# Optimization experiments

Measured on AMD Instinct MI355X. Metric: run time of the kernel, lower is better.

Reference implementation:

```python
import jax, jax.numpy as jnp
import numpy as np

DIM = 1024
HEADS = 16
HEAD_DIM = DIM // HEADS
SCALE = HEAD_DIM ** -0.5


def setup_inputs() -> dict:
    key = jax.random.key(0)
    ks = jax.random.split(key, 9)
    b, n, m = 4, 1024, 1024
    x = jax.random.normal(ks[0], (b, n, DIM), dtype=jnp.float32)
    context = jax.random.normal(ks[1], (b, m, DIM), dtype=jnp.float32)
    mask = jax.random.randint(ks[2], (b, n, 32, 32), 0, 2, dtype=jnp.int32)
    s = DIM ** -0.5
    Wq = jax.random.normal(ks[3], (DIM, DIM), dtype=jnp.float32) * s
    bq = jnp.zeros((DIM,), dtype=jnp.float32)
    Wkv = jax.random.normal(ks[4], (DIM, 2 * DIM), dtype=jnp.float32) * s
    bkv = jnp.zeros((2 * DIM,), dtype=jnp.float32)
    Wp = jax.random.normal(ks[5], (DIM, DIM), dtype=jnp.float32) * s
    bp = jnp.zeros((DIM,), dtype=jnp.float32)
    return {"x": x, "context": context, "mask": mask,
            "Wq": Wq, "bq": bq, "Wkv": Wkv, "bkv": bkv, "Wp": Wp, "bp": bp}


def reference(x, context, mask, Wq, bq, Wkv, bkv, Wp, bp):
    b, n, _ = x.shape
    m = context.shape[1]
    h, d = HEADS, HEAD_DIM
    # projections
    q = (x @ Wq + bq).reshape(b, n, h, d).transpose(0, 2, 1, 3)       # [b,h,n,d]
    kv = (context @ Wkv + bkv).reshape(b, m, 2, h, d)
    k = kv[:, :, 0].transpose(0, 2, 1, 3)                              # [b,h,m,d]
    v = kv[:, :, 1].transpose(0, 2, 1, 3)                              # [b,h,m,d]
    dots = jnp.einsum('bhnd,bhmd->bhnm', q, k) * SCALE                 # [b,h,n,m]
    # mask: [b,n,H,W] -> [b,1,n,m]; masked_fill where mask == 0
    mflat = mask.reshape(b, n, m)[:, None]                             # [b,1,n,m]
    dots = jnp.where(mflat == 0, -jnp.inf, dots)
    attn = jax.nn.softmax(dots, axis=-1)
    out = jnp.einsum('bhnm,bhmd->bhnd', attn, v)
    out = out.transpose(0, 2, 1, 3).reshape(b, n, h * d)
    return out @ Wp + bp
```

## Files before the change

### kernel.cpp

```cpp
#include <hip/hip_runtime.h>
#include <type_traits>

typedef __bf16 bf16;
typedef __bf16 bf16x8 __attribute__((ext_vector_type(8)));
typedef float f32x4 __attribute__((ext_vector_type(4)));
typedef unsigned long long u64;

#define MFMA16(a, b, c) __builtin_amdgcn_mfma_f32_16x16x32_bf16(a, b, c, 0, 0, 0)

__global__ __launch_bounds__(256)
void transpose_weights_k(const float* __restrict__ Wq,
                         const float* __restrict__ Wkv,
                         const float* __restrict__ Wp,
                         bf16* __restrict__ BqkvT, bf16* __restrict__ WpT) {
  const int ct = blockIdx.x, rt = blockIdx.y;
  const float* src;
  bf16* dst;
  int C, c0, drow0;
  if (ct < 16) {
    src = Wq; C = 1024; c0 = ct * 64; dst = BqkvT; drow0 = c0;
  } else if (ct < 48) {
    src = Wkv; C = 2048; c0 = (ct - 16) * 64; dst = BqkvT; drow0 = 1024 + c0;
  } else {
    src = Wp; C = 1024; c0 = (ct - 48) * 64; dst = WpT; drow0 = c0;
  }
  __shared__ bf16 T[64][72];
  const int tid = threadIdx.x;
  const int r0 = rt * 64;
#pragma unroll
  for (int i = 0; i < 2; ++i) {
    int c = i * 256 + tid;
    int row = c >> 3, col = (c & 7) * 8;
    const float* sp = &src[(size_t)(r0 + row) * C + c0 + col];
    f32x4 a0 = *(const f32x4*)sp;
    f32x4 a1 = *(const f32x4*)(sp + 4);
    bf16x8 t;
#pragma unroll
    for (int j = 0; j < 4; ++j) { t[j] = (bf16)a0[j]; t[4 + j] = (bf16)a1[j]; }
    *(bf16x8*)&T[row][col] = t;
  }
  __syncthreads();
#pragma unroll
  for (int i = 0; i < 2; ++i) {
    int c = i * 256 + tid;
    int orow = c >> 3, ocol = (c & 7) * 8;
    bf16x8 v;
#pragma unroll
    for (int j = 0; j < 8; ++j) v[j] = T[ocol + j][orow];
    *(bf16x8*)&dst[(size_t)(drow0 + orow) * 1024 + r0 + ocol] = v;
  }
}

__global__ __launch_bounds__(256)
void maskpack_k(const int* __restrict__ mask, u64* __restrict__ out) {
  const int idx = blockIdx.x * 256 + threadIdx.x;
  const int4* p = (const int4*)(mask + (size_t)idx * 64);
  u64 v = 0;
#pragma unroll
  for (int i = 0; i < 16; ++i) {
    int4 m = p[i];
    v |= (u64)(m.x != 0) << (4 * i);
    v |= (u64)(m.y != 0) << (4 * i + 1);
    v |= (u64)(m.z != 0) << (4 * i + 2);
    v |= (u64)(m.w != 0) << (4 * i + 3);
  }
  out[idx] = v;
}

template <int EPI, typename TA>
__global__ __launch_bounds__(256)
void gemm64x128(const TA* __restrict__ A0, const TA* __restrict__ A1,
                const bf16* __restrict__ Bt, const float* __restrict__ bias0,
                const float* __restrict__ bias1, bf16* __restrict__ oq,
                bf16* __restrict__ ok, bf16* __restrict__ ovt,
                float* __restrict__ out0f, int K) {
  __shared__ bf16 As[64][72];
  __shared__ bf16 Bs[128][72];
  const int tid = threadIdx.x;
  const int lane = tid & 63;
  const int w = tid >> 6;
  const int wm = (w >> 1) * 32, wn = (w & 1) * 64;
  const int l15 = lane & 15, l4 = lane >> 4;
  const int n0g = blockIdx.x * 128;
  const int m0 = blockIdx.y * 64;

  const TA* A = (EPI == 1 && n0g >= 1024) ? A1 : A0;

  const int ar = tid >> 2, ac0 = (tid & 3) * 16;
  const int br = tid >> 1, bc0 = (tid & 1) * 32;

  f32x4 acc[2][4] = {};

  for (int kk = 0; kk < K; kk += 64) {
    if constexpr (std::is_same_v<TA, float>) {
      const float* ap = &A[(size_t)(m0 + ar) * K + kk + ac0];
#pragma unroll
      for (int half = 0; half < 2; ++half) {
        f32x4 a0 = *(const f32x4*)(ap + half * 8);
        f32x4 a1 = *(const f32x4*)(ap + half * 8 + 4);
        bf16x8 t;
#pragma unroll
        for (int j = 0; j < 4; ++j) { t[j] = (bf16)a0[j]; t[4 + j] = (bf16)a1[j]; }
        *(bf16x8*)&As[ar][ac0 + half * 8] = t;
      }
    } else {
      const bf16* ap = &A[(size_t)(m0 + ar) * K + kk + ac0];
      *(bf16x8*)&As[ar][ac0] = *(const bf16x8*)ap;
      *(bf16x8*)&As[ar][ac0 + 8] = *(const bf16x8*)(ap + 8);
    }
    {
      const bf16* bp = &Bt[(size_t)(n0g + br) * K + kk + bc0];
#pragma unroll
      for (int half = 0; half < 4; ++half)
        *(bf16x8*)&Bs[br][bc0 + half * 8] = *(const bf16x8*)(bp + half * 8);
    }
    __syncthreads();
#pragma unroll
    for (int ks = 0; ks < 2; ++ks) {
      bf16x8 af[2], bfr[4];
#pragma unroll
      for (int i = 0; i < 2; ++i)
        af[i] = *(const bf16x8*)&As[wm + i * 16 + l15][ks * 32 + l4 * 8];
#pragma unroll
      for (int j = 0; j < 4; ++j)
        bfr[j] = *(const bf16x8*)&Bs[wn + j * 16 + l15][ks * 32 + l4 * 8];
#pragma unroll
      for (int i = 0; i < 2; ++i)
#pragma unroll
        for (int j = 0; j < 4; ++j)
          acc[i][j] = MFMA16(af[i], bfr[j], acc[i][j]);
    }
    __syncthreads();
  }

  const float SCALE2 = 0.18033688011112042f;
#pragma unroll
  for (int j = 0; j < 4; ++j) {
    const int col = n0g + wn + j * 16 + l15;
    float bc;
    if (EPI == 1) bc = (col < 1024) ? bias0[col] : bias1[col - 1024];
    else bc = bias0[col];
#pragma unroll
    for (int i = 0; i < 2; ++i) {
#pragma unroll
      for (int r = 0; r < 4; ++r) {
        const int row = m0 + wm + i * 16 + l4 * 4 + r;
        const float v = acc[i][j][r] + bc;
        if (EPI == 0) {
          out0f[(size_t)row * 1024 + col] = v;
        } else {
          const int b = row >> 10, n = row & 1023;
          if (col < 1024) {
            const int h = col >> 6, d = col & 63;
            oq[(((size_t)(b * 16 + h)) * 1024 + n) * 64 + d] =
                (bf16)(v * SCALE2);
          } else {
            const int ckv = col - 1024;
            const int s = ckv >> 10, c2 = ckv & 1023;
            const int h = c2 >> 6, d = c2 & 63;
            if (s == 0)
              ok[(((size_t)(b * 16 + h)) * 1024 + n) * 64 + d] = (bf16)v;
            else
              ovt[(((size_t)(b * 16 + h)) * 64 + d) * 1024 + n] = (bf16)v;
          }
        }
      }
    }
  }
}

__global__ __launch_bounds__(256)
void attn_kernel(const bf16* __restrict__ q, const bf16* __restrict__ k,
                 const bf16* __restrict__ vT, const u64* __restrict__ maskbits,
                 bf16* __restrict__ ao) {
  const int ntile = blockIdx.x;
  const int bh = blockIdx.y;
  const int b = bh >> 4, h = bh & 15;
  const int tid = threadIdx.x;
  const int lane = tid & 63;
  const int w = tid >> 6;
  const int l15 = lane & 15, l4 = lane >> 4;

  __shared__ bf16 Ks[64][72];
  __shared__ bf16 Vts[64][72];
  __shared__ bf16 Pw[4][16][72];

  const size_t base = (size_t)bh * 65536;
  const int nrow0 = ntile * 64 + w * 16;

  bf16x8 qf[2];
#pragma unroll
  for (int ks = 0; ks < 2; ++ks)
    qf[ks] =
        *(const bf16x8*)&q[base + (size_t)(nrow0 + l15) * 64 + ks * 32 + l4 * 8];

  f32x4 o[4] = {};
  float lsum[4] = {0.0f, 0.0f, 0.0f, 0.0f};

  const u64* mb = maskbits + (size_t)(b * 1024 + nrow0) * 16;

  for (int mt = 0; mt < 16; ++mt) {
#pragma unroll
    for (int i = 0; i < 2; ++i) {
      int c = i * 256 + tid;
      int row = c >> 3, col = (c & 7) * 8;
      *(bf16x8*)&Ks[row][col] =
          *(const bf16x8*)&k[base + (size_t)(mt * 64 + row) * 64 + col];
      *(bf16x8*)&Vts[row][col] =
          *(const bf16x8*)&vT[base + (size_t)row * 1024 + mt * 64 + col];
    }
    __syncthreads();

    f32x4 s[4];
#pragma unroll
    for (int sub = 0; sub < 4; ++sub) s[sub] = f32x4{-12.f, -12.f, -12.f, -12.f};
#pragma unroll
    for (int ks = 0; ks < 2; ++ks) {
#pragma unroll
      for (int sub = 0; sub < 4; ++sub) {
        bf16x8 bfr = *(const bf16x8*)&Ks[sub * 16 + l15][ks * 32 + l4 * 8];
        s[sub] = MFMA16(qf[ks], bfr, s[sub]);
      }
    }

    u64 wbits[4];
#pragma unroll
    for (int r = 0; r < 4; ++r) wbits[r] = mb[(size_t)(l4 * 4 + r) * 16 + mt];

#pragma unroll
    for (int sub = 0; sub < 4; ++sub) {
#pragma unroll
      for (int r = 0; r < 4; ++r) {
        float p = exp2f(s[sub][r]);
        p = ((wbits[r] >> (sub * 16 + l15)) & 1) ? p : 0.0f;
        lsum[r] += p;
        Pw[w][l4 * 4 + r][sub * 16 + l15] = (bf16)p;
      }
    }

#pragma unroll
    for (int ks = 0; ks < 2; ++ks) {
      bf16x8 af = *(const bf16x8*)&Pw[w][l15][ks * 32 + l4 * 8];
#pragma unroll
      for (int sub = 0; sub < 4; ++sub) {
        bf16x8 bfr = *(const bf16x8*)&Vts[sub * 16 + l15][ks * 32 + l4 * 8];
        o[sub] = MFMA16(af, bfr, o[sub]);
      }
    }
    __syncthreads();
  }

  float inv[4];
#pragma unroll
  for (int r = 0; r < 4; ++r) {
    float t = lsum[r];
#pragma unroll
    for (int d = 1; d < 16; d <<= 1) t += __shfl_xor(t, d);
    inv[r] = 1.0f / t;
  }

#pragma unroll
  for (int sub = 0; sub < 4; ++sub) {
#pragma unroll
    for (int r = 0; r < 4; ++r) {
      const int n = nrow0 + l4 * 4 + r;
      const size_t idx =
          ((size_t)(b * 1024 + n)) * 1024 + h * 64 + sub * 16 + l15;
      ao[idx] = (bf16)(o[sub][r] * inv[r]);
    }
  }
}

extern "C" void kernel_launch(void* const* d_in, const int* in_sizes, int n_in,
                              void* d_out, int out_size, void* d_ws,
                              size_t ws_size, hipStream_t stream) {
  const float* x = (const float*)d_in[0];
  const float* context = (const float*)d_in[1];
  const int* mask = (const int*)d_in[2];
  const float* Wq = (const float*)d_in[3];
  const float* bq = (const float*)d_in[4];
  const float* Wkv = (const float*)d_in[5];
  const float* bkv = (const float*)d_in[6];
  const float* Wp = (const float*)d_in[7];
  const float* bp = (const float*)d_in[8];
  float* out = (float*)d_out;

  char* ws = (char*)d_ws;
  bf16* BqkvT = (bf16*)(ws);
  u64* maskbits = (u64*)(ws);
  bf16* WpT = (bf16*)(ws + (6ull << 20));
  bf16* qw = (bf16*)(ws + (8ull << 20));
  bf16* kw = (bf16*)(ws + (16ull << 20));
  bf16* vtw = (bf16*)(ws + (24ull << 20));
  bf16* aow = (bf16*)(ws + (32ull << 20));

  const dim3 blk(256);

  transpose_weights_k<<<dim3(64, 16), blk, 0, stream>>>(Wq, Wkv, Wp, BqkvT,
                                                        WpT);

  gemm64x128<1, float><<<dim3(24, 64), blk, 0, stream>>>(
      x, context, BqkvT, bq, bkv, qw, kw, vtw, nullptr, 1024);

  maskpack_k<<<dim3(256), blk, 0, stream>>>(mask, maskbits);

  attn_kernel<<<dim3(16, 64), blk, 0, stream>>>(qw, kw, vtw, maskbits, aow);

  gemm64x128<0, bf16><<<dim3(8, 64), blk, 0, stream>>>(
      aow, nullptr, WpT, bp, nullptr, nullptr, nullptr, nullptr, out, 1024);
}
```

Before: 249.6 us.

## Use direct global-to-LDS loads and larger QKV GEMM tiles with bf16 context precast

```diff
diff --git a/kernel.cpp b/kernel.cpp
--- a/kernel.cpp
+++ b/kernel.cpp
@@ -1,5 +1,4 @@
 #include <hip/hip_runtime.h>
-#include <type_traits>
 
 typedef __bf16 bf16;
 typedef __bf16 bf16x8 __attribute__((ext_vector_type(8)));
@@ -8,12 +7,30 @@
 
 #define MFMA16(a, b, c) __builtin_amdgcn_mfma_f32_16x16x32_bf16(a, b, c, 0, 0, 0)
 
+__device__ __forceinline__ void gl_lds16(const void* g, void* l) {
+  __builtin_amdgcn_global_load_lds(
+      (const __attribute__((address_space(1))) unsigned int*)g,
+      (__attribute__((address_space(3))) unsigned int*)l, 16, 0, 0);
+}
+
+__global__ __launch_bounds__(256)
+void cvt_f32_bf16_k(const float* __restrict__ src, bf16* __restrict__ dst) {
+  const size_t i = ((size_t)blockIdx.x * 256 + threadIdx.x) * 8;
+  f32x4 a0 = *(const f32x4*)(src + i);
+  f32x4 a1 = *(const f32x4*)(src + i + 4);
+  bf16x8 t;
+#pragma unroll
+  for (int j = 0; j < 4; ++j) { t[j] = (bf16)a0[j]; t[4 + j] = (bf16)a1[j]; }
+  *(bf16x8*)(dst + i) = t;
+}
+
 __global__ __launch_bounds__(256)
 void transpose_weights_k(const float* __restrict__ Wq,
                          const float* __restrict__ Wkv,
                          const float* __restrict__ Wp,
-                         bf16* __restrict__ BqkvT, bf16* __restrict__ WpT) {
-  const int ct = blockIdx.x, rt = blockIdx.y;
+                         bf16* __restrict__ BqkvT, bf16* __restrict__ WpT,
+                         int ct_off) {
+  const int ct = blockIdx.x + ct_off, rt = blockIdx.y;
   const float* src;
   bf16* dst;
   int C, c0, drow0;
@@ -67,52 +84,125 @@
   out[idx] = v;
 }
 
-template <int EPI, typename TA>
-__global__ __launch_bounds__(256)
-void gemm64x128(const TA* __restrict__ A0, const TA* __restrict__ A1,
-                const bf16* __restrict__ Bt, const float* __restrict__ bias0,
-                const float* __restrict__ bias1, bf16* __restrict__ oq,
-                bf16* __restrict__ ok, bf16* __restrict__ ovt,
-                float* __restrict__ out0f, int K) {
-  __shared__ bf16 As[64][72];
-  __shared__ bf16 Bs[128][72];
+__global__ __launch_bounds__(256)
+void gemm_qkv(const float* __restrict__ xf, const bf16* __restrict__ cb,
+              const bf16* __restrict__ Bt, const float* __restrict__ bq,
+              const float* __restrict__ bkv, bf16* __restrict__ oq,
+              bf16* __restrict__ ok, bf16* __restrict__ ovt) {
+  __shared__ bf16 As[128][64];
+  __shared__ bf16 Bs[128][64];
+  const int tid = threadIdx.x;
+  const int lane = tid & 63;
+  const int w = tid >> 6;
+  const int wm = (w >> 1) * 64, wn = (w & 1) * 64;
+  const int l15 = lane & 15, l4 = lane >> 4;
+  const int lrow = lane >> 3, lcol = (lane & 7) * 8;
+  const int n0g = blockIdx.x * 128;
+  const int m0 = blockIdx.y * 128;
+  const bool qside = (n0g < 1024);
+
+  const int ar = tid >> 1, ac0 = (tid & 1) * 32;
+
+  f32x4 acc[4][4] = {};
+
+  for (int kk = 0; kk < 1024; kk += 64) {
+#pragma unroll
+    for (int it = 0; it < 4; ++it) {
+      const int r = w * 32 + it * 8;
+      gl_lds16(&Bt[(size_t)(n0g + r + lrow) * 1024 + kk + lcol], &Bs[r][0]);
+    }
+    if (qside) {
+      const float* ap = &xf[(size_t)(m0 + ar) * 1024 + kk + ac0];
+#pragma unroll
+      for (int h = 0; h < 4; ++h) {
+        f32x4 a0 = *(const f32x4*)(ap + h * 8);
+        f32x4 a1 = *(const f32x4*)(ap + h * 8 + 4);
+        bf16x8 t;
+#pragma unroll
+        for (int j = 0; j < 4; ++j) { t[j] = (bf16)a0[j]; t[4 + j] = (bf16)a1[j]; }
+        *(bf16x8*)&As[ar][ac0 + h * 8] = t;
+      }
+    } else {
+#pragma unroll
+      for (int it = 0; it < 4; ++it) {
+        const int r = w * 32 + it * 8;
+        gl_lds16(&cb[(size_t)(m0 + r + lrow) * 1024 + kk + lcol], &As[r][0]);
+      }
+    }
+    __syncthreads();
+#pragma unroll
+    for (int ks = 0; ks < 2; ++ks) {
+      bf16x8 af[4], bfr[4];
+#pragma unroll
+      for (int i = 0; i < 4; ++i)
+        af[i] = *(const bf16x8*)&As[wm + i * 16 + l15][ks * 32 + l4 * 8];
+#pragma unroll
+      for (int j = 0; j < 4; ++j)
+        bfr[j] = *(const bf16x8*)&Bs[wn + j * 16 + l15][ks * 32 + l4 * 8];
+#pragma unroll
+      for (int i = 0; i < 4; ++i)
+#pragma unroll
+        for (int j = 0; j < 4; ++j)
+          acc[i][j] = MFMA16(af[i], bfr[j], acc[i][j]);
+    }
+    __syncthreads();
+  }
+
+  const float SCALE2 = 0.18033688011112042f;
+#pragma unroll
+  for (int j = 0; j < 4; ++j) {
+    const int col = n0g + wn + j * 16 + l15;
+    const float bc = (col < 1024) ? bq[col] : bkv[col - 1024];
+#pragma unroll
+    for (int i = 0; i < 4; ++i) {
+#pragma unroll
+      for (int r = 0; r < 4; ++r) {
+        const int row = m0 + wm + i * 16 + l4 * 4 + r;
+        const float v = acc[i][j][r] + bc;
+        const int b = row >> 10, n = row & 1023;
+        if (col < 1024) {
+          const int h = col >> 6, d = col & 63;
+          oq[(((size_t)(b * 16 + h)) * 1024 + n) * 64 + d] = (bf16)(v * SCALE2);
+        } else {
+          const int ckv = col - 1024;
+          const int s = ckv >> 10, c2 = ckv & 1023;
+          const int h = c2 >> 6, d = c2 & 63;
+          if (s == 0)
+            ok[(((size_t)(b * 16 + h)) * 1024 + n) * 64 + d] = (bf16)v;
+          else
+            ovt[(((size_t)(b * 16 + h)) * 64 + d) * 1024 + n] = (bf16)v;
+        }
+      }
+    }
+  }
+}
+
+__global__ __launch_bounds__(256)
+void gemm_op(const bf16* __restrict__ A, const bf16* __restrict__ Bt,
+             const float* __restrict__ bias, float* __restrict__ out) {
+  __shared__ bf16 As[64][64];
+  __shared__ bf16 Bs[128][64];
   const int tid = threadIdx.x;
   const int lane = tid & 63;
   const int w = tid >> 6;
   const int wm = (w >> 1) * 32, wn = (w & 1) * 64;
   const int l15 = lane & 15, l4 = lane >> 4;
-  const int n0g = blockIdx.x * 128;
+  const int lrow = lane >> 3, lcol = (lane & 7) * 8;
+  const int n0 = blockIdx.x * 128;
   const int m0 = blockIdx.y * 64;
 
-  const TA* A = (EPI == 1 && n0g >= 1024) ? A1 : A0;
-
-  const int ar = tid >> 2, ac0 = (tid & 3) * 16;
-  const int br = tid >> 1, bc0 = (tid & 1) * 32;
-
   f32x4 acc[2][4] = {};
 
-  for (int kk = 0; kk < K; kk += 64) {
-    if constexpr (std::is_same_v<TA, float>) {
-      const float* ap = &A[(size_t)(m0 + ar) * K + kk + ac0];
-#pragma unroll
-      for (int half = 0; half < 2; ++half) {
-        f32x4 a0 = *(const f32x4*)(ap + half * 8);
-        f32x4 a1 = *(const f32x4*)(ap + half * 8 + 4);
-        bf16x8 t;
-#pragma unroll
-        for (int j = 0; j < 4; ++j) { t[j] = (bf16)a0[j]; t[4 + j] = (bf16)a1[j]; }
-        *(bf16x8*)&As[ar][ac0 + half * 8] = t;
-      }
-    } else {
-      const bf16* ap = &A[(size_t)(m0 + ar) * K + kk + ac0];
-      *(bf16x8*)&As[ar][ac0] = *(const bf16x8*)ap;
-      *(bf16x8*)&As[ar][ac0 + 8] = *(const bf16x8*)(ap + 8);
-    }
-    {
-      const bf16* bp = &Bt[(size_t)(n0g + br) * K + kk + bc0];
-#pragma unroll
-      for (int half = 0; half < 4; ++half)
-        *(bf16x8*)&Bs[br][bc0 + half * 8] = *(const bf16x8*)(bp + half * 8);
+  for (int kk = 0; kk < 1024; kk += 64) {
+#pragma unroll
+    for (int it = 0; it < 4; ++it) {
+      const int r = w * 32 + it * 8;
+      gl_lds16(&Bt[(size_t)(n0 + r + lrow) * 1024 + kk + lcol], &Bs[r][0]);
+    }
+#pragma unroll
+    for (int it = 0; it < 2; ++it) {
+      const int r = w * 16 + it * 8;
+      gl_lds16(&A[(size_t)(m0 + r + lrow) * 1024 + kk + lcol], &As[r][0]);
     }
     __syncthreads();
 #pragma unroll
@@ -133,37 +223,16 @@
     __syncthreads();
   }
 
-  const float SCALE2 = 0.18033688011112042f;
 #pragma unroll
   for (int j = 0; j < 4; ++j) {
-    const int col = n0g + wn + j * 16 + l15;
-    float bc;
-    if (EPI == 1) bc = (col < 1024) ? bias0[col] : bias1[col - 1024];
-    else bc = bias0[col];
+    const int col = n0 + wn + j * 16 + l15;
+    const float bc = bias[col];
 #pragma unroll
     for (int i = 0; i < 2; ++i) {
 #pragma unroll
       for (int r = 0; r < 4; ++r) {
         const int row = m0 + wm + i * 16 + l4 * 4 + r;
-        const float v = acc[i][j][r] + bc;
-        if (EPI == 0) {
-          out0f[(size_t)row * 1024 + col] = v;
-        } else {
-          const int b = row >> 10, n = row & 1023;
-          if (col < 1024) {
-            const int h = col >> 6, d = col & 63;
-            oq[(((size_t)(b * 16 + h)) * 1024 + n) * 64 + d] =
-                (bf16)(v * SCALE2);
-          } else {
-            const int ckv = col - 1024;
-            const int s = ckv >> 10, c2 = ckv & 1023;
-            const int h = c2 >> 6, d = c2 & 63;
-            if (s == 0)
-              ok[(((size_t)(b * 16 + h)) * 1024 + n) * 64 + d] = (bf16)v;
-            else
-              ovt[(((size_t)(b * 16 + h)) * 64 + d) * 1024 + n] = (bf16)v;
-          }
-        }
+        out[(size_t)row * 1024 + col] = acc[i][j][r] + bc;
       }
     }
   }
@@ -286,26 +355,30 @@
   float* out = (float*)d_out;
 
   char* ws = (char*)d_ws;
-  bf16* BqkvT = (bf16*)(ws);
-  u64* maskbits = (u64*)(ws);
-  bf16* WpT = (bf16*)(ws + (6ull << 20));
-  bf16* qw = (bf16*)(ws + (8ull << 20));
-  bf16* kw = (bf16*)(ws + (16ull << 20));
-  bf16* vtw = (bf16*)(ws + (24ull << 20));
-  bf16* aow = (bf16*)(ws + (32ull << 20));
+  bf16* cb = (bf16*)(ws);
+  bf16* aow = (bf16*)(ws);
+  bf16* BqkvT = (bf16*)(ws + (8ull << 20));
+  u64* maskbits = (u64*)(ws + (8ull << 20));
+  bf16* WpT = (bf16*)(ws + (9ull << 20));
+  bf16* qw = (bf16*)(ws + (14ull << 20));
+  bf16* kw = (bf16*)(ws + (22ull << 20));
+  bf16* vtw = (bf16*)(ws + (30ull << 20));
 
   const dim3 blk(256);
 
-  transpose_weights_k<<<dim3(64, 16), blk, 0, stream>>>(Wq, Wkv, Wp, BqkvT,
-                                                        WpT);
-
-  gemm64x128<1, float><<<dim3(24, 64), blk, 0, stream>>>(
-      x, context, BqkvT, bq, bkv, qw, kw, vtw, nullptr, 1024);
+  cvt_f32_bf16_k<<<dim3(2048), blk, 0, stream>>>(context, cb);
+
+  transpose_weights_k<<<dim3(48, 16), blk, 0, stream>>>(Wq, Wkv, Wp, BqkvT,
+                                                        WpT, 0);
+
+  gemm_qkv<<<dim3(24, 32), blk, 0, stream>>>(x, cb, BqkvT, bq, bkv, qw, kw,
+                                             vtw);
 
   maskpack_k<<<dim3(256), blk, 0, stream>>>(mask, maskbits);
+  transpose_weights_k<<<dim3(16, 16), blk, 0, stream>>>(Wq, Wkv, Wp, BqkvT,
+                                                        WpT, 48);
 
   attn_kernel<<<dim3(16, 64), blk, 0, stream>>>(qw, kw, vtw, maskbits, aow);
 
-  gemm64x128<0, bf16><<<dim3(8, 64), blk, 0, stream>>>(
-      aow, nullptr, WpT, bp, nullptr, nullptr, nullptr, nullptr, out, 1024);
-}
+  gemm_op<<<dim3(8, 64), blk, 0, stream>>>(aow, WpT, bp, out);
+}
```

Measured after the change: 269.3 us. 7.9% more time.

## Merge prep kernels and use direct global-to-LDS loads with XOR-swizzled GEMM tiles

Applied to the files above, without the earlier changes.

```diff
diff --git a/kernel.cpp b/kernel.cpp
--- a/kernel.cpp
+++ b/kernel.cpp
@@ -1,5 +1,4 @@
 #include <hip/hip_runtime.h>
-#include <type_traits>
 
 typedef __bf16 bf16;
 typedef __bf16 bf16x8 __attribute__((ext_vector_type(8)));
@@ -8,12 +7,35 @@
 
 #define MFMA16(a, b, c) __builtin_amdgcn_mfma_f32_16x16x32_bf16(a, b, c, 0, 0, 0)
 
+__device__ __forceinline__ void gl_lds16(const void* g, void* l) {
+  __builtin_amdgcn_global_load_lds(
+      (const __attribute__((address_space(1))) unsigned int*)g,
+      (__attribute__((address_space(3))) unsigned int*)l, 16, 0, 0);
+}
+
 __global__ __launch_bounds__(256)
-void transpose_weights_k(const float* __restrict__ Wq,
-                         const float* __restrict__ Wkv,
-                         const float* __restrict__ Wp,
-                         bf16* __restrict__ BqkvT, bf16* __restrict__ WpT) {
-  const int ct = blockIdx.x, rt = blockIdx.y;
+void prep_k(const float* __restrict__ Wq, const float* __restrict__ Wkv,
+            const float* __restrict__ Wp, const int* __restrict__ mask,
+            bf16* __restrict__ BqkvT, bf16* __restrict__ WpT,
+            u64* __restrict__ maskbits) {
+  const int bx = blockIdx.x;
+  const int tid = threadIdx.x;
+  if (bx >= 1024) {
+    const int idx = (bx - 1024) * 256 + tid;
+    const int4* p = (const int4*)(mask + (size_t)idx * 64);
+    u64 v = 0;
+#pragma unroll
+    for (int i = 0; i < 16; ++i) {
+      int4 m = p[i];
+      v |= (u64)(m.x != 0) << (4 * i);
+      v |= (u64)(m.y != 0) << (4 * i + 1);
+      v |= (u64)(m.z != 0) << (4 * i + 2);
+      v |= (u64)(m.w != 0) << (4 * i + 3);
+    }
+    maskbits[idx] = v;
+    return;
+  }
+  const int ct = bx >> 4, rt = bx & 15;
   const float* src;
   bf16* dst;
   int C, c0, drow0;
@@ -25,7 +47,6 @@
     src = Wp; C = 1024; c0 = (ct - 48) * 64; dst = WpT; drow0 = c0;
   }
   __shared__ bf16 T[64][72];
-  const int tid = threadIdx.x;
   const int r0 = rt * 64;
 #pragma unroll
   for (int i = 0; i < 2; ++i) {
@@ -51,79 +72,68 @@
   }
 }
 
+template <int EPI>
 __global__ __launch_bounds__(256)
-void maskpack_k(const int* __restrict__ mask, u64* __restrict__ out) {
-  const int idx = blockIdx.x * 256 + threadIdx.x;
-  const int4* p = (const int4*)(mask + (size_t)idx * 64);
-  u64 v = 0;
-#pragma unroll
-  for (int i = 0; i < 16; ++i) {
-    int4 m = p[i];
-    v |= (u64)(m.x != 0) << (4 * i);
-    v |= (u64)(m.y != 0) << (4 * i + 1);
-    v |= (u64)(m.z != 0) << (4 * i + 2);
-    v |= (u64)(m.w != 0) << (4 * i + 3);
-  }
-  out[idx] = v;
-}
-
-template <int EPI, typename TA>
-__global__ __launch_bounds__(256)
-void gemm64x128(const TA* __restrict__ A0, const TA* __restrict__ A1,
-                const bf16* __restrict__ Bt, const float* __restrict__ bias0,
-                const float* __restrict__ bias1, bf16* __restrict__ oq,
-                bf16* __restrict__ ok, bf16* __restrict__ ovt,
-                float* __restrict__ out0f, int K) {
-  __shared__ bf16 As[64][72];
-  __shared__ bf16 Bs[128][72];
+void gemm_sw(const float* __restrict__ Af0, const float* __restrict__ Af1,
+             const bf16* __restrict__ Ab, const bf16* __restrict__ Bt,
+             const float* __restrict__ bias0, const float* __restrict__ bias1,
+             bf16* __restrict__ oq, bf16* __restrict__ ok,
+             bf16* __restrict__ ovt, float* __restrict__ outf) {
+  __shared__ bf16 As[64][64];
+  __shared__ bf16 Bs[128][64];
   const int tid = threadIdx.x;
   const int lane = tid & 63;
   const int w = tid >> 6;
   const int wm = (w >> 1) * 32, wn = (w & 1) * 64;
   const int l15 = lane & 15, l4 = lane >> 4;
-  const int n0g = blockIdx.x * 128;
+  const int lrow = lane >> 3;
+  const int scol = ((lane & 7) ^ (lrow & 7)) * 8;
+  const int n0 = blockIdx.x * 128;
   const int m0 = blockIdx.y * 64;
 
-  const TA* A = (EPI == 1 && n0g >= 1024) ? A1 : A0;
-
-  const int ar = tid >> 2, ac0 = (tid & 3) * 16;
-  const int br = tid >> 1, bc0 = (tid & 1) * 32;
+  const float* Asrc = (EPI == 1) ? ((n0 < 1024) ? Af0 : Af1) : nullptr;
+
+  const int ar = tid >> 2;
+  const int acb = (tid & 3) * 2;
 
   f32x4 acc[2][4] = {};
 
-  for (int kk = 0; kk < K; kk += 64) {
-    if constexpr (std::is_same_v<TA, float>) {
-      const float* ap = &A[(size_t)(m0 + ar) * K + kk + ac0];
-#pragma unroll
-      for (int half = 0; half < 2; ++half) {
-        f32x4 a0 = *(const f32x4*)(ap + half * 8);
-        f32x4 a1 = *(const f32x4*)(ap + half * 8 + 4);
+  for (int kk = 0; kk < 1024; kk += 64) {
+#pragma unroll
+    for (int it = 0; it < 4; ++it) {
+      const int r = w * 32 + it * 8;
+      gl_lds16(&Bt[(size_t)(n0 + r + lrow) * 1024 + kk + scol], &Bs[r][0]);
+    }
+    if (EPI == 0) {
+#pragma unroll
+      for (int it = 0; it < 2; ++it) {
+        const int r = w * 16 + it * 8;
+        gl_lds16(&Ab[(size_t)(m0 + r + lrow) * 1024 + kk + scol], &As[r][0]);
+      }
+    } else {
+#pragma unroll
+      for (int j = 0; j < 2; ++j) {
+        const int cbL = acb + j;
+        const float* ap = &Asrc[(size_t)(m0 + ar) * 1024 + kk + cbL * 8];
+        f32x4 a0 = *(const f32x4*)ap;
+        f32x4 a1 = *(const f32x4*)(ap + 4);
         bf16x8 t;
 #pragma unroll
-        for (int j = 0; j < 4; ++j) { t[j] = (bf16)a0[j]; t[4 + j] = (bf16)a1[j]; }
-        *(bf16x8*)&As[ar][ac0 + half * 8] = t;
-      }
-    } else {
-      const bf16* ap = &A[(size_t)(m0 + ar) * K + kk + ac0];
-      *(bf16x8*)&As[ar][ac0] = *(const bf16x8*)ap;
-      *(bf16x8*)&As[ar][ac0 + 8] = *(const bf16x8*)(ap + 8);
-    }
-    {
-      const bf16* bp = &Bt[(size_t)(n0g + br) * K + kk + bc0];
-#pragma unroll
-      for (int half = 0; half < 4; ++half)
-        *(bf16x8*)&Bs[br][bc0 + half * 8] = *(const bf16x8*)(bp + half * 8);
+        for (int u = 0; u < 4; ++u) { t[u] = (bf16)a0[u]; t[4 + u] = (bf16)a1[u]; }
+        *(bf16x8*)&As[ar][(cbL ^ (ar & 7)) * 8] = t;
+      }
     }
     __syncthreads();
 #pragma unroll
     for (int ks = 0; ks < 2; ++ks) {
+      const int sw = ((ks * 4 + l4) ^ (l15 & 7)) * 8;
       bf16x8 af[2], bfr[4];
 #pragma unroll
       for (int i = 0; i < 2; ++i)
-        af[i] = *(const bf16x8*)&As[wm + i * 16 + l15][ks * 32 + l4 * 8];
+        af[i] = *(const bf16x8*)&As[wm + i * 16 + l15][sw];
 #pragma unroll
       for (int j = 0; j < 4; ++j)
-        bfr[j] = *(const bf16x8*)&Bs[wn + j * 16 + l15][ks * 32 + l4 * 8];
+        bfr[j] = *(const bf16x8*)&Bs[wn + j * 16 + l15][sw];
 #pragma unroll
       for (int i = 0; i < 2; ++i)
 #pragma unroll
@@ -136,7 +146,7 @@
   const float SCALE2 = 0.18033688011112042f;
 #pragma unroll
   for (int j = 0; j < 4; ++j) {
-    const int col = n0g + wn + j * 16 + l15;
+    const int col = n0 + wn + j * 16 + l15;
     float bc;
     if (EPI == 1) bc = (col < 1024) ? bias0[col] : bias1[col - 1024];
     else bc = bias0[col];
@@ -147,7 +157,7 @@
         const int row = m0 + wm + i * 16 + l4 * 4 + r;
         const float v = acc[i][j][r] + bc;
         if (EPI == 0) {
-          out0f[(size_t)row * 1024 + col] = v;
+          outf[(size_t)row * 1024 + col] = v;
         } else {
           const int b = row >> 10, n = row & 1023;
           if (col < 1024) {
@@ -287,25 +297,24 @@
 
   char* ws = (char*)d_ws;
   bf16* BqkvT = (bf16*)(ws);
-  u64* maskbits = (u64*)(ws);
-  bf16* WpT = (bf16*)(ws + (6ull << 20));
+  bf16* aow = (bf16*)(ws);
   bf16* qw = (bf16*)(ws + (8ull << 20));
   bf16* kw = (bf16*)(ws + (16ull << 20));
   bf16* vtw = (bf16*)(ws + (24ull << 20));
-  bf16* aow = (bf16*)(ws + (32ull << 20));
+  u64* maskbits = (u64*)(ws + (32ull << 20));
+  bf16* WpT = (bf16*)(ws + (33ull << 20));
 
   const dim3 blk(256);
 
-  transpose_weights_k<<<dim3(64, 16), blk, 0, stream>>>(Wq, Wkv, Wp, BqkvT,
-                                                        WpT);
-
-  gemm64x128<1, float><<<dim3(24, 64), blk, 0, stream>>>(
-      x, context, BqkvT, bq, bkv, qw, kw, vtw, nullptr, 1024);
-
-  maskpack_k<<<dim3(256), blk, 0, stream>>>(mask, maskbits);
+  prep_k<<<dim3(1280), blk, 0, stream>>>(Wq, Wkv, Wp, mask, BqkvT, WpT,
+                                         maskbits);
+
+  gemm_sw<1><<<dim3(24, 64), blk, 0, stream>>>(x, context, nullptr, BqkvT, bq,
+                                               bkv, qw, kw, vtw, nullptr);
 
   attn_kernel<<<dim3(16, 64), blk, 0, stream>>>(qw, kw, vtw, maskbits, aow);
 
-  gemm64x128<0, bf16><<<dim3(8, 64), blk, 0, stream>>>(
-      aow, nullptr, WpT, bp, nullptr, nullptr, nullptr, nullptr, out, 1024);
-}
+  gemm_sw<0><<<dim3(8, 64), blk, 0, stream>>>(nullptr, nullptr, aow, WpT, bp,
+                                              nullptr, nullptr, nullptr,
+                                              nullptr, out);
+}
```

Measured after the change: 241.2 us. 3.4% less time.
